# Kernel optimization log

Hardware: AMD Instinct MI355X
Metric: run time of the kernel (lower is better)

Reference implementation:

```python
import jax, jax.numpy as jnp
import numpy as np

B, L, F, P = 128, 256, 4, 4   # dialogs, dialog length, future/past links
IN, H, C = 1024, 256, 7
N = B * L


def _build_edges():
    # same structure as build_intra_graph: self-loop + F future + P past per node
    i = np.arange(L)
    ss, tt = [], []
    for d in range(-P, F + 1):
        j = i + d
        m = (j >= 0) & (j < L)
        ss.append(i[m]); tt.append(j[m])
    s = np.concatenate(ss); t = np.concatenate(tt)
    offs = (np.arange(B) * L)[:, None]
    S = (s[None, :] + offs).ravel()
    T = (t[None, :] + offs).ravel()
    return np.stack([S, T]).astype(np.int32)


def setup_inputs() -> dict:
    key = jax.random.key(0)
    ks = jax.random.split(key, 16)
    ei = _build_edges()
    speakers = np.asarray(jax.random.randint(ks[0], (N,), 0, 2), dtype=np.int32)
    rel = (speakers[ei[0]] * speakers[ei[1]]).astype(np.int32)
    sd_in = 1.0 / np.sqrt(IN)
    sd_h = 1.0 / np.sqrt(H)
    return {
        "input": jax.random.normal(ks[1], (N, IN), jnp.float32),
        "dialog_lengths": jnp.full((B,), L, jnp.int32),
        "speakers": jnp.asarray(speakers),
        "labels": jax.random.randint(ks[2], (N,), 0, C, jnp.int32),
        "edge_index": jnp.asarray(ei),
        "rel_type": jnp.asarray(rel),
        # RGCNConv(IN, H, num_relations=2): per-relation weight, root weight, bias
        "W_rgcn": jax.random.normal(ks[3], (2, IN, H), jnp.float32) * sd_in,
        "W_root": jax.random.normal(ks[4], (IN, H), jnp.float32) * sd_in,
        "b_rgcn": jax.random.normal(ks[5], (H,), jnp.float32) * 0.01,
        # GraphConv(H, H): lin_rel (on aggregated neighbors, with bias), lin_root (no bias)
        "W_rel": jax.random.normal(ks[6], (H, H), jnp.float32) * sd_h,
        "b_rel": jax.random.normal(ks[7], (H,), jnp.float32) * 0.01,
        "W_grt": jax.random.normal(ks[8], (H, H), jnp.float32) * sd_h,
        # skip_con: Linear(IN, H)
        "W_skip": jax.random.normal(ks[9], (IN, H), jnp.float32) * sd_in,
        "b_skip": jax.random.normal(ks[10], (H,), jnp.float32) * 0.01,
        # classify: Linear(H, C)
        "W_cls": jax.random.normal(ks[11], (H, C), jnp.float32) * sd_h,
        "b_cls": jax.random.normal(ks[12], (C,), jnp.float32) * 0.01,
    }


def reference(input, dialog_lengths, speakers, labels, edge_index, rel_type,
              W_rgcn, W_root, b_rgcn, W_rel, b_rel, W_grt,
              W_skip, b_skip, W_cls, b_cls):
    n = input.shape[0]
    src, dst = edge_index[0], edge_index[1]
    seg = jax.ops.segment_sum

    # --- RGCNConv: out_i = x_i @ W_root + b + sum_r mean_{j in N_r(i)} x_j @ W_r
    t = jnp.einsum('ni,rio->rno', input, W_rgcn)      # [2, N, H]
    msg = t[rel_type, src]                            # [E, H] relation-specific messages
    h = input @ W_root + b_rgcn
    for r in range(2):
        m = (rel_type == r).astype(input.dtype)       # [E]
        s = seg(msg * m[:, None], dst, num_segments=n)
        cnt = seg(m, dst, num_segments=n)
        h = h + s / jnp.maximum(cnt, 1.0)[:, None]    # mean aggregation per relation

    # --- GraphConv (aggr='add'): out_i = W_rel @ sum_j h_j + b_rel + W_grt @ h_i
    neigh = seg(h[src], dst, num_segments=n)          # [N, H]
    h2 = neigh @ W_rel + b_rel + h @ W_grt

    # --- skip connection + classifier
    out = (h2 + input @ W_skip + b_skip) @ W_cls + b_cls  # [N, C]

    # --- cross entropy (mean)
    logp = jax.nn.log_softmax(out, axis=-1)
    loss = -jnp.mean(jnp.take_along_axis(logp, labels[:, None].astype(jnp.int32), axis=1))
    return out, loss
```

## Files before the change

### kernel.cpp

```cpp
#include <hip/hip_runtime.h>

#define NN 32768
#define INF 1024
#define HF 256

typedef __bf16 bf16x8 __attribute__((ext_vector_type(8)));
typedef float f32x4 __attribute__((ext_vector_type(4)));
typedef unsigned short u16x8 __attribute__((ext_vector_type(8)));

__device__ __forceinline__ float bf2f(unsigned short u) {
  union { unsigned int i; float f; } v; v.i = ((unsigned int)u) << 16; return v.f;
}
__device__ __forceinline__ unsigned short f2bf(float f) {
  union { float f; unsigned int i; } v; v.f = f;
  unsigned int x = v.i;
  return (unsigned short)((x + 0x7fffu + ((x >> 16) & 1u)) >> 16);
}

__device__ __forceinline__ void ld_lds16(const unsigned short* g, unsigned short* l) {
  __builtin_amdgcn_global_load_lds(
      (__attribute__((address_space(1))) const unsigned int*)g,
      (__attribute__((address_space(3))) unsigned int*)l, 16, 0, 0);
}

__global__ __launch_bounds__(256)
void diagcn_prep(const float* __restrict__ x, const float* __restrict__ Wrgcn,
                 const float* __restrict__ Wroot, const float* __restrict__ Wskip,
                 const float* __restrict__ Wgrt, const float* __restrict__ Wrel,
                 unsigned short* __restrict__ Xbf, unsigned short* __restrict__ WbigT,
                 unsigned short* __restrict__ WsmT, float* __restrict__ loss) {
  int bid = blockIdx.x;
  if (bid < 32768) {
    if (bid == 0 && threadIdx.x == 0) loss[0] = 0.f;
    int idx = bid * 256 + threadIdx.x;
    float4 v = ((const float4*)x)[idx];
    ushort4 u; u.x = f2bf(v.x); u.y = f2bf(v.y); u.z = f2bf(v.z); u.w = f2bf(v.w);
    ((ushort4*)Xbf)[idx] = u;
    return;
  }
  __shared__ float tile[64 * 65];
  int tb = bid - 32768;
  const float* src;
  int k0, ncol0;
  unsigned short* dst;
  int ldd, nrow0;
  if (tb < 256) {
    int tn = tb >> 4, tk = tb & 15;
    int mat = tn >> 2;
    src = (mat == 0) ? Wrgcn : (mat == 1) ? (Wrgcn + 262144) : (mat == 2) ? Wroot : Wskip;
    k0 = tk * 64; ncol0 = (tn & 3) * 64;
    dst = WbigT; ldd = 1024; nrow0 = tn * 64;
  } else {
    int t2 = tb - 256;
    int tn = t2 >> 3, tk = t2 & 7;
    src = (tk < 4) ? Wgrt : Wrel;
    k0 = (tk & 3) * 64; ncol0 = tn * 64;
    dst = WsmT; ldd = 512; nrow0 = tn * 64;
  }
  int kdst0 = (tb < 256) ? k0 : (((tb - 256) & 7) * 64);
  int c = threadIdx.x & 63, rb = threadIdx.x >> 6;
#pragma unroll
  for (int it = 0; it < 16; ++it) {
    int r = rb + it * 4;
    tile[r * 65 + c] = src[(size_t)(k0 + r) * 256 + ncol0 + c];
  }
  __syncthreads();
  int kk = threadIdx.x & 63;
#pragma unroll
  for (int it = 0; it < 16; ++it) {
    int nn = rb + it * 4;
    dst[(size_t)(nrow0 + nn) * ldd + kdst0 + kk] = f2bf(tile[kk * 65 + nn]);
  }
}

template<bool STG, int VM, bool LAST>
__device__ __forceinline__ void g1_tile(int t,
    const unsigned short* __restrict__ gA0, const unsigned short* __restrict__ gB0,
    unsigned short* SH, int w, int abase, int bbase, int sw8,
    bf16x8 (&av)[4], bf16x8 (&bv)[4], bf16x8 (&nav)[4], bf16x8 (&nbv)[4],
    f32x4 (&acc)[8][4]) {
  unsigned short* Ab = SH + ((t & 3) << 14);
  unsigned short* Bb = Ab + 8192;
  bf16x8 av2[4];
#pragma unroll
  for (int i = 0; i < 4; ++i)
    av2[i] = *(const bf16x8*)&Ab[(abase + 64 + i * 16) * 32 + sw8];
  __builtin_amdgcn_sched_barrier(0);
  if (STG) {
    unsigned short* dA = SH + (((t + 3) & 3) << 14) + (w << 10);
    const unsigned short* gA = gA0 + (t + 3) * 32;
    ld_lds16(gA, dA);
    ld_lds16(gA + 16 * 1024, dA + 512);
    unsigned short* dB = SH + (((t + 3) & 3) << 14) + 8192 + (w << 10);
    const unsigned short* gB = gB0 + (t + 3) * 32;
    ld_lds16(gB, dB);
    ld_lds16(gB + 16 * 1024, dB + 512);
  }
  asm volatile("s_waitcnt lgkmcnt(4)");
  __builtin_amdgcn_sched_barrier(0);
  __builtin_amdgcn_s_setprio(1);
#pragma unroll
  for (int i = 0; i < 4; ++i)
#pragma unroll
    for (int j = 0; j < 4; ++j)
      acc[i][j] = __builtin_amdgcn_mfma_f32_16x16x32_bf16(av[i], bv[j], acc[i][j], 0, 0, 0);
  __builtin_amdgcn_s_setprio(0);
  __builtin_amdgcn_sched_barrier(0);
  if constexpr (VM == 8) asm volatile("s_waitcnt vmcnt(8)" ::: "memory");
  else if constexpr (VM == 4) asm volatile("s_waitcnt vmcnt(4)" ::: "memory");
  else if constexpr (VM == 0) asm volatile("s_waitcnt vmcnt(0)" ::: "memory");
  __builtin_amdgcn_s_barrier();
  if constexpr (!LAST) {
    unsigned short* An = SH + (((t + 1) & 3) << 14);
    unsigned short* Bn = An + 8192;
#pragma unroll
    for (int i = 0; i < 4; ++i)
      nav[i] = *(const bf16x8*)&An[(abase + i * 16) * 32 + sw8];
    __builtin_amdgcn_sched_barrier(0);
    asm volatile("s_waitcnt lgkmcnt(4)");
    __builtin_amdgcn_sched_barrier(0);
    __builtin_amdgcn_s_setprio(1);
#pragma unroll
    for (int i = 0; i < 2; ++i)
#pragma unroll
      for (int j = 0; j < 4; ++j)
        acc[4 + i][j] = __builtin_amdgcn_mfma_f32_16x16x32_bf16(av2[i], bv[j], acc[4 + i][j], 0, 0, 0);
    __builtin_amdgcn_s_setprio(0);
    __builtin_amdgcn_sched_barrier(0);
#pragma unroll
    for (int j = 0; j < 4; ++j)
      nbv[j] = *(const bf16x8*)&Bn[(bbase + j * 16) * 32 + sw8];
    __builtin_amdgcn_sched_barrier(0);
    __builtin_amdgcn_s_setprio(1);
#pragma unroll
    for (int i = 2; i < 4; ++i)
#pragma unroll
      for (int j = 0; j < 4; ++j)
        acc[4 + i][j] = __builtin_amdgcn_mfma_f32_16x16x32_bf16(av2[i], bv[j], acc[4 + i][j], 0, 0, 0);
    __builtin_amdgcn_s_setprio(0);
    __builtin_amdgcn_s_barrier();
  } else {
    asm volatile("s_waitcnt lgkmcnt(0)");
    __builtin_amdgcn_sched_barrier(0);
#pragma unroll
    for (int i = 0; i < 4; ++i)
#pragma unroll
      for (int j = 0; j < 4; ++j)
        acc[4 + i][j] = __builtin_amdgcn_mfma_f32_16x16x32_bf16(av2[i], bv[j], acc[4 + i][j], 0, 0, 0);
  }
}

__global__ __launch_bounds__(512, 2)
void diagcn_gemm1(const unsigned short* __restrict__ A, const unsigned short* __restrict__ BT,
                  unsigned short* __restrict__ Y) {
  __shared__ unsigned short SH[65536];
  const int tid = threadIdx.x;
  const int w = tid >> 6, lane = tid & 63;
  const int quad = lane >> 4, l15 = lane & 15;
  const int wm = w >> 2, wn = w & 3;
  const int b = blockIdx.x;
  const int wg = ((b & 7) << 6) + (b >> 3);
  const int m0 = (wg >> 2) << 8;
  const int n0 = (wg & 3) << 8;
  const int abase = wm * 128 + l15;
  const int bbase = wn * 64 + l15;
  const int sw8 = ((quad ^ ((l15 >> 1) & 3)) << 3);
  const int csrc8 = (((lane & 3) ^ ((lane >> 3) & 3)) << 3);
  const unsigned short* gA0 = A + (size_t)(m0 + w * 32 + (lane >> 2)) * 1024 + csrc8;
  const unsigned short* gB0 = BT + (size_t)(n0 + w * 32 + (lane >> 2)) * 1024 + csrc8;

  f32x4 acc[8][4] = {};
  bf16x8 avA[4], bvA[4], avB[4], bvB[4];

#pragma unroll
  for (int tt = 0; tt < 3; ++tt) {
    unsigned short* dA = SH + (tt << 14) + (w << 10);
    ld_lds16(gA0 + tt * 32, dA);
    ld_lds16(gA0 + tt * 32 + 16 * 1024, dA + 512);
    unsigned short* dB = SH + (tt << 14) + 8192 + (w << 10);
    ld_lds16(gB0 + tt * 32, dB);
    ld_lds16(gB0 + tt * 32 + 16 * 1024, dB + 512);
  }
  asm volatile("s_waitcnt vmcnt(8)" ::: "memory");
  __builtin_amdgcn_s_barrier();
#pragma unroll
  for (int i = 0; i < 4; ++i)
    avA[i] = *(const bf16x8*)&SH[(abase + i * 16) * 32 + sw8];
#pragma unroll
  for (int j = 0; j < 4; ++j)
    bvA[j] = *(const bf16x8*)&SH[8192 + (bbase + j * 16) * 32 + sw8];
  __builtin_amdgcn_sched_barrier(0);

#pragma unroll 1
  for (int tt = 0; tt < 14; ++tt) {
    g1_tile<true, 8, false>(2 * tt, gA0, gB0, SH, w, abase, bbase, sw8,
                            avA, bvA, avB, bvB, acc);
    g1_tile<true, 8, false>(2 * tt + 1, gA0, gB0, SH, w, abase, bbase, sw8,
                            avB, bvB, avA, bvA, acc);
  }
  g1_tile<true, 8, false>(28, gA0, gB0, SH, w, abase, bbase, sw8, avA, bvA, avB, bvB, acc);
  g1_tile<false, 4, false>(29, gA0, gB0, SH, w, abase, bbase, sw8, avB, bvB, avA, bvA, acc);
  g1_tile<false, 0, false>(30, gA0, gB0, SH, w, abase, bbase, sw8, avA, bvA, avB, bvB, acc);
  g1_tile<false, -1, true>(31, gA0, gB0, SH, w, abase, bbase, sw8, avB, bvB, avA, bvA, acc);

#pragma unroll
  for (int i = 0; i < 8; ++i)
#pragma unroll
    for (int j = 0; j < 4; ++j) {
      const int row = m0 + wm * 128 + i * 16 + quad * 4;
      const int col = n0 + wn * 64 + j * 16 + l15;
#pragma unroll
      for (int r = 0; r < 4; ++r)
        Y[(size_t)(row + r) * 1024 + col] = f2bf(acc[i][j][r]);
    }
}

__global__ __launch_bounds__(256)
void diagcn_hn(const unsigned short* __restrict__ Y, const int* __restrict__ spk,
               const float* __restrict__ brgcn, unsigned short* __restrict__ A2) {
  __shared__ unsigned short hbuf[72 * 256];
  int b = blockIdx.x;
  int node0 = ((b & 7) << 12) + ((b >> 3) << 6);
  int d0 = node0 & ~255;
  int wv = threadIdx.x >> 6, lane = threadIdx.x & 63;
  int half = lane >> 5, li = lane & 31, c0 = li << 3;
  int slot = wv * 2 + half;

#pragma unroll 1
  for (int pass = 0; pass < 9; ++pass) {
    int idx = pass * 8 + slot;
    int src = node0 - 4 + idx;
    int sc = src < d0 ? d0 : (src > d0 + 255 ? d0 + 255 : src);
    int p = sc & 255;
    int si = spk[sc];
    float a0[8] = {}, a1[8] = {};
    float n0 = 0.f, n1 = 0.f;
#pragma unroll
    for (int d = -4; d <= 4; ++d) {
      int pj = p + d;
      float w = (pj >= 0 && pj < 256) ? 1.f : 0.f;
      int jc = pj < 0 ? 0 : (pj > 255 ? 255 : pj);
      int nj = d0 + jc;
      int rel = si & spk[nj];
      u16x8 v = *(const u16x8*)&Y[(size_t)nj * 1024 + (rel << 8) + c0];
      float w1 = rel ? w : 0.f, w0 = rel ? 0.f : w;
#pragma unroll
      for (int k = 0; k < 8; ++k) {
        float f = bf2f(v[k]);
        a0[k] += f * w0; a1[k] += f * w1;
      }
      n0 += w0; n1 += w1;
    }
    u16x8 vr = *(const u16x8*)&Y[(size_t)sc * 1024 + 512 + c0];
    float i0 = 1.f / fmaxf(n0, 1.f), i1 = 1.f / fmaxf(n1, 1.f);
    u16x8 u;
#pragma unroll
    for (int k = 0; k < 8; ++k)
      u[k] = f2bf(bf2f(vr[k]) + brgcn[c0 + k] + a0[k] * i0 + a1[k] * i1);
    *(u16x8*)&hbuf[idx * 256 + c0] = u;
    if (idx >= 4 && idx < 68)
      *(u16x8*)&A2[(size_t)(node0 + idx - 4) * 512 + c0] = u;
  }
  __syncthreads();

#pragma unroll 1
  for (int pass = 0; pass < 8; ++pass) {
    int idx = pass * 8 + slot;
    int node = node0 + idx;
    int p = node & 255;
    float s[8] = {};
#pragma unroll
    for (int d = -4; d <= 4; ++d) {
      int pj = p + d;
      float w = (pj >= 0 && pj < 256) ? 1.f : 0.f;
      int lidx = idx + 4 + d;
      u16x8 v = *(const u16x8*)&hbuf[lidx * 256 + c0];
#pragma unroll
      for (int k = 0; k < 8; ++k) s[k] += bf2f(v[k]) * w;
    }
    u16x8 u;
#pragma unroll
    for (int k = 0; k < 8; ++k) u[k] = f2bf(s[k]);
    *(u16x8*)&A2[(size_t)node * 512 + 256 + c0] = u;
  }
}

__global__ __launch_bounds__(256)
void diagcn_gemm2(const unsigned short* __restrict__ A, const unsigned short* __restrict__ BT,
                  const unsigned short* __restrict__ Y, const float* __restrict__ Wcls,
                  const float* __restrict__ bcls, const float* __restrict__ brel,
                  const float* __restrict__ bskip, const int* __restrict__ labels,
                  float* __restrict__ out, float* __restrict__ loss) {
  const int K = 512;
  __shared__ unsigned short As[64 * 64];
  __shared__ unsigned short Bs[256 * 64];
  __shared__ float Wc[2312];
  for (int i = threadIdx.x; i < 2312; i += 256) {
    float v;
    if (i < 1792) v = Wcls[i];
    else if (i < 1799) v = bcls[i - 1792];
    else if (i < 1800) v = 0.f;
    else if (i < 2056) v = brel[i - 1800];
    else v = bskip[i - 2056];
    Wc[i] = v;
  }
  const int tid = threadIdx.x;
  const int w = tid >> 6, lane = tid & 63;
  const int quad = lane >> 4, l15 = lane & 15;
  const int b = blockIdx.x;
  const int m0 = (((b & 7) << 6) + (b >> 3)) << 6;
  const int rowg = lane >> 3;
  const int kbsw = (lane & 7) ^ rowg;

  f32x4 acc[16] = {};
  const unsigned short* Abase = A + (size_t)m0 * K + kbsw * 8;
  const unsigned short* Bbase = BT + kbsw * 8;

  for (int k0 = 0; k0 < K; k0 += 64) {
#pragma unroll
    for (int t = 0; t < 2; ++t) {
      int grp = w * 2 + t;
      ld_lds16(Abase + (size_t)(grp * 8 + rowg) * K + k0, &As[grp * 512]);
    }
#pragma unroll
    for (int t = 0; t < 8; ++t) {
      int grp = w * 8 + t;
      ld_lds16(Bbase + (size_t)(grp * 8 + rowg) * K + k0, &Bs[grp * 512]);
    }
    __syncthreads();
#pragma unroll
    for (int ks = 0; ks < 2; ++ks) {
      int kb = ks * 4 + quad;
      int ra = w * 16 + l15;
      bf16x8 av = *(const bf16x8*)&As[ra * 64 + ((kb ^ (ra & 7)) << 3)];
#pragma unroll
      for (int j = 0; j < 16; ++j) {
        int rb2 = j * 16 + l15;
        bf16x8 bv = *(const bf16x8*)&Bs[rb2 * 64 + ((kb ^ (rb2 & 7)) << 3)];
        acc[j] = __builtin_amdgcn_mfma_f32_16x16x32_bf16(av, bv, acc[j], 0, 0, 0);
      }
    }
    __syncthreads();
  }

  float wsum[4][7] = {};
#pragma unroll
  for (int j = 0; j < 16; ++j) {
    int col = j * 16 + l15;
    float bb = Wc[1800 + col] + Wc[2056 + col];
#pragma unroll
    for (int r = 0; r < 4; ++r) {
      int row = m0 + w * 16 + quad * 4 + r;
      float z = acc[j][r] + bb + bf2f(Y[(size_t)row * 1024 + 768 + col]);
#pragma unroll
      for (int c = 0; c < 7; ++c) wsum[r][c] += z * Wc[col * 7 + c];
    }
  }
#pragma unroll
  for (int o = 1; o < 16; o <<= 1)
#pragma unroll
    for (int r = 0; r < 4; ++r)
#pragma unroll
      for (int c = 0; c < 7; ++c) wsum[r][c] += __shfl_xor(wsum[r][c], o, 64);

  float lsum = 0.f;
#pragma unroll
  for (int r = 0; r < 4; ++r) {
    int row = m0 + w * 16 + quad * 4 + r;
    float o7[7], mx = -1e30f;
#pragma unroll
    for (int c = 0; c < 7; ++c) {
      o7[c] = wsum[r][c] + Wc[1792 + c];
      mx = fmaxf(mx, o7[c]);
    }
    if (l15 < 7) out[(size_t)row * 7 + l15] = o7[l15];
    float s = 0.f;
#pragma unroll
    for (int c = 0; c < 7; ++c) s += expf(o7[c] - mx);
    int lab = labels[row];
    lsum += mx + logf(s) - o7[lab];
  }
  lsum += __shfl_xor(lsum, 16, 64);
  lsum += __shfl_xor(lsum, 32, 64);
  if (lane == 0) atomicAdd(loss, lsum * (1.0f / (float)NN));
}

extern "C" void kernel_launch(void* const* d_in, const int* in_sizes, int n_in,
                              void* d_out, int out_size, void* d_ws, size_t ws_size,
                              hipStream_t stream) {
  const float* x      = (const float*)d_in[0];
  const int* speakers = (const int*)d_in[2];
  const int* labels   = (const int*)d_in[3];
  const float* Wrgcn  = (const float*)d_in[6];
  const float* Wroot  = (const float*)d_in[7];
  const float* brgcn  = (const float*)d_in[8];
  const float* Wrel   = (const float*)d_in[9];
  const float* brel   = (const float*)d_in[10];
  const float* Wgrt   = (const float*)d_in[11];
  const float* Wskip  = (const float*)d_in[12];
  const float* bskip  = (const float*)d_in[13];
  const float* Wcls   = (const float*)d_in[14];
  const float* bcls   = (const float*)d_in[15];
  float* out = (float*)d_out;
  float* loss = out + (size_t)NN * 7;

  const size_t OFF_XBF  = 0;
  const size_t OFF_WBIG = 67108864;
  const size_t OFF_WSM  = 69206016;
  const size_t OFF_Y    = 69468160;
  const size_t OFF_A2   = 136577024;
  const size_t NEED     = 170131456;
  if (ws_size < NEED) return;

  char* ws = (char*)d_ws;
  unsigned short* Xbf   = (unsigned short*)(ws + OFF_XBF);
  unsigned short* WbigT = (unsigned short*)(ws + OFF_WBIG);
  unsigned short* WsmT  = (unsigned short*)(ws + OFF_WSM);
  unsigned short* Y     = (unsigned short*)(ws + OFF_Y);
  unsigned short* A2    = (unsigned short*)(ws + OFF_A2);

  diagcn_prep<<<dim3(33056), dim3(256), 0, stream>>>(x, Wrgcn, Wroot, Wskip, Wgrt, Wrel,
                                                     Xbf, WbigT, WsmT, loss);
  diagcn_gemm1<<<dim3(512), dim3(512), 0, stream>>>(Xbf, WbigT, Y);
  diagcn_hn<<<dim3(512), dim3(256), 0, stream>>>(Y, speakers, brgcn, A2);
  diagcn_gemm2<<<dim3(512), dim3(256), 0, stream>>>(A2, WsmT, Y, Wcls, bcls, brel, bskip,
                                                    labels, out, loss);
}
```

Baseline: 369.1 us.

## Fuse fp32-to-bf16 input conversion into GEMM1 A-tile staging

Removes the separate pass that converted the 32768x1024 fp32 input to bf16 in workspace. GEMM1 now loads fp32 A tiles into registers two stages ahead, converts them to bf16 and writes them to LDS itself, while B tiles still use direct global-to-LDS loads. This avoids writing and rereading a 64 MB bf16 copy, at the cost of twice the global read bytes for A inside the GEMM, extra VGPRs and conversion ALU work in the pipelined loop, and reworked waitcnt accounting.

```diff
diff --git a/kernel.cpp b/kernel.cpp
--- a/kernel.cpp
+++ b/kernel.cpp
@@ -24,22 +24,13 @@
 }
 
 __global__ __launch_bounds__(256)
-void diagcn_prep(const float* __restrict__ x, const float* __restrict__ Wrgcn,
-                 const float* __restrict__ Wroot, const float* __restrict__ Wskip,
-                 const float* __restrict__ Wgrt, const float* __restrict__ Wrel,
-                 unsigned short* __restrict__ Xbf, unsigned short* __restrict__ WbigT,
+void diagcn_prep(const float* __restrict__ Wrgcn, const float* __restrict__ Wroot,
+                 const float* __restrict__ Wskip, const float* __restrict__ Wgrt,
+                 const float* __restrict__ Wrel, unsigned short* __restrict__ WbigT,
                  unsigned short* __restrict__ WsmT, float* __restrict__ loss) {
-  int bid = blockIdx.x;
-  if (bid < 32768) {
-    if (bid == 0 && threadIdx.x == 0) loss[0] = 0.f;
-    int idx = bid * 256 + threadIdx.x;
-    float4 v = ((const float4*)x)[idx];
-    ushort4 u; u.x = f2bf(v.x); u.y = f2bf(v.y); u.z = f2bf(v.z); u.w = f2bf(v.w);
-    ((ushort4*)Xbf)[idx] = u;
-    return;
-  }
+  int tb = blockIdx.x;
+  if (tb == 0 && threadIdx.x == 0) loss[0] = 0.f;
   __shared__ float tile[64 * 65];
-  int tb = bid - 32768;
   const float* src;
   int k0, ncol0;
   unsigned short* dst;
@@ -73,30 +64,48 @@
   }
 }
 
-template<bool STG, int VM, bool LAST>
+template<bool WR, bool LDA, bool LDB, int VM, bool LAST>
 __device__ __forceinline__ void g1_tile(int t,
-    const unsigned short* __restrict__ gA0, const unsigned short* __restrict__ gB0,
-    unsigned short* SH, int w, int abase, int bbase, int sw8,
+    const float* __restrict__ gAf, const unsigned short* __restrict__ gB0,
+    unsigned short* SH, int w, int lane, int abase, int bbase, int sw8,
     bf16x8 (&av)[4], bf16x8 (&bv)[4], bf16x8 (&nav)[4], bf16x8 (&nbv)[4],
-    f32x4 (&acc)[8][4]) {
+    f32x4 (&sreg)[4], f32x4 (&acc)[8][4]) {
   unsigned short* Ab = SH + ((t & 3) << 14);
   unsigned short* Bb = Ab + 8192;
+  if constexpr (VM == 2) asm volatile("s_waitcnt vmcnt(2)" ::: "memory");
+  else if constexpr (VM == 0) asm volatile("s_waitcnt vmcnt(0)" ::: "memory");
+  if constexpr (WR) {
+    unsigned short* dA = SH + (((t + 2) & 3) << 14) + (w << 10) + lane * 8;
+    u16x8 p0, p1;
+#pragma unroll
+    for (int k = 0; k < 4; ++k) {
+      p0[k] = f2bf(sreg[0][k]); p0[4 + k] = f2bf(sreg[1][k]);
+      p1[k] = f2bf(sreg[2][k]); p1[4 + k] = f2bf(sreg[3][k]);
+    }
+    *(u16x8*)dA = p0;
+    *(u16x8*)(dA + 512) = p1;
+  }
+  __builtin_amdgcn_sched_barrier(0);
   bf16x8 av2[4];
 #pragma unroll
   for (int i = 0; i < 4; ++i)
     av2[i] = *(const bf16x8*)&Ab[(abase + 64 + i * 16) * 32 + sw8];
   __builtin_amdgcn_sched_barrier(0);
-  if (STG) {
-    unsigned short* dA = SH + (((t + 3) & 3) << 14) + (w << 10);
-    const unsigned short* gA = gA0 + (t + 3) * 32;
-    ld_lds16(gA, dA);
-    ld_lds16(gA + 16 * 1024, dA + 512);
+  if constexpr (LDA) {
+    const float* g = gAf + (t + 3) * 32;
+    sreg[0] = *(const f32x4*)g;
+    sreg[1] = *(const f32x4*)(g + 4);
+    sreg[2] = *(const f32x4*)(g + 16384);
+    sreg[3] = *(const f32x4*)(g + 16388);
+  }
+  if constexpr (LDB) {
     unsigned short* dB = SH + (((t + 3) & 3) << 14) + 8192 + (w << 10);
     const unsigned short* gB = gB0 + (t + 3) * 32;
     ld_lds16(gB, dB);
     ld_lds16(gB + 16 * 1024, dB + 512);
   }
-  asm volatile("s_waitcnt lgkmcnt(4)");
+  if constexpr (WR) asm volatile("s_waitcnt lgkmcnt(6)");
+  else              asm volatile("s_waitcnt lgkmcnt(4)");
   __builtin_amdgcn_sched_barrier(0);
   __builtin_amdgcn_s_setprio(1);
 #pragma unroll
@@ -105,10 +114,6 @@
     for (int j = 0; j < 4; ++j)
       acc[i][j] = __builtin_amdgcn_mfma_f32_16x16x32_bf16(av[i], bv[j], acc[i][j], 0, 0, 0);
   __builtin_amdgcn_s_setprio(0);
-  __builtin_amdgcn_sched_barrier(0);
-  if constexpr (VM == 8) asm volatile("s_waitcnt vmcnt(8)" ::: "memory");
-  else if constexpr (VM == 4) asm volatile("s_waitcnt vmcnt(4)" ::: "memory");
-  else if constexpr (VM == 0) asm volatile("s_waitcnt vmcnt(0)" ::: "memory");
   __builtin_amdgcn_s_barrier();
   if constexpr (!LAST) {
     unsigned short* An = SH + (((t + 1) & 3) << 14);
@@ -151,7 +156,7 @@
 }
 
 __global__ __launch_bounds__(512, 2)
-void diagcn_gemm1(const unsigned short* __restrict__ A, const unsigned short* __restrict__ BT,
+void diagcn_gemm1(const float* __restrict__ X, const unsigned short* __restrict__ BT,
                   unsigned short* __restrict__ Y) {
   __shared__ unsigned short SH[65536];
   const int tid = threadIdx.x;
@@ -166,22 +171,54 @@
   const int bbase = wn * 64 + l15;
   const int sw8 = ((quad ^ ((l15 >> 1) & 3)) << 3);
   const int csrc8 = (((lane & 3) ^ ((lane >> 3) & 3)) << 3);
-  const unsigned short* gA0 = A + (size_t)(m0 + w * 32 + (lane >> 2)) * 1024 + csrc8;
+  const float* gAf = X + (size_t)(m0 + w * 32 + (lane >> 2)) * 1024 + csrc8;
   const unsigned short* gB0 = BT + (size_t)(n0 + w * 32 + (lane >> 2)) * 1024 + csrc8;
 
   f32x4 acc[8][4] = {};
+  f32x4 sreg[4];
   bf16x8 avA[4], bvA[4], avB[4], bvB[4];
 
-#pragma unroll
-  for (int tt = 0; tt < 3; ++tt) {
-    unsigned short* dA = SH + (tt << 14) + (w << 10);
-    ld_lds16(gA0 + tt * 32, dA);
-    ld_lds16(gA0 + tt * 32 + 16 * 1024, dA + 512);
-    unsigned short* dB = SH + (tt << 14) + 8192 + (w << 10);
-    ld_lds16(gB0 + tt * 32, dB);
-    ld_lds16(gB0 + tt * 32 + 16 * 1024, dB + 512);
+  {
+    unsigned short* dA = SH + (w << 10) + lane * 8;
+#pragma unroll
+    for (int tt = 0; tt < 2; ++tt) {
+      const float* g = gAf + tt * 32;
+      sreg[0] = *(const f32x4*)g;
+      sreg[1] = *(const f32x4*)(g + 4);
+      sreg[2] = *(const f32x4*)(g + 16384);
+      sreg[3] = *(const f32x4*)(g + 16388);
+      asm volatile("s_waitcnt vmcnt(0)" ::: "memory");
+      u16x8 p0, p1;
+#pragma unroll
+      for (int k = 0; k < 4; ++k) {
+        p0[k] = f2bf(sreg[0][k]); p0[4 + k] = f2bf(sreg[1][k]);
+        p1[k] = f2bf(sreg[2][k]); p1[4 + k] = f2bf(sreg[3][k]);
+      }
+      unsigned short* d = dA + tt * 16384;
+      *(u16x8*)d = p0;
+      *(u16x8*)(d + 512) = p1;
+    }
+#pragma unroll
+    for (int tt = 0; tt < 2; ++tt) {
+      unsigned short* dB = SH + (tt << 14) + 8192 + (w << 10);
+      ld_lds16(gB0 + tt * 32, dB);
+      ld_lds16(gB0 + tt * 32 + 16 * 1024, dB + 512);
+    }
+    {
+      const float* g = gAf + 2 * 32;
+      sreg[0] = *(const f32x4*)g;
+      sreg[1] = *(const f32x4*)(g + 4);
+      sreg[2] = *(const f32x4*)(g + 16384);
+      sreg[3] = *(const f32x4*)(g + 16388);
+    }
+    {
+      unsigned short* dB = SH + (2 << 14) + 8192 + (w << 10);
+      ld_lds16(gB0 + 2 * 32, dB);
+      ld_lds16(gB0 + 2 * 32 + 16 * 1024, dB + 512);
+    }
   }
   asm volatile("s_waitcnt vmcnt(8)" ::: "memory");
+  asm volatile("s_waitcnt lgkmcnt(0)");
   __builtin_amdgcn_s_barrier();
 #pragma unroll
   for (int i = 0; i < 4; ++i)
@@ -193,15 +230,19 @@
 
 #pragma unroll 1
   for (int tt = 0; tt < 14; ++tt) {
-    g1_tile<true, 8, false>(2 * tt, gA0, gB0, SH, w, abase, bbase, sw8,
-                            avA, bvA, avB, bvB, acc);
-    g1_tile<true, 8, false>(2 * tt + 1, gA0, gB0, SH, w, abase, bbase, sw8,
-                            avB, bvB, avA, bvA, acc);
-  }
-  g1_tile<true, 8, false>(28, gA0, gB0, SH, w, abase, bbase, sw8, avA, bvA, avB, bvB, acc);
-  g1_tile<false, 4, false>(29, gA0, gB0, SH, w, abase, bbase, sw8, avB, bvB, avA, bvA, acc);
-  g1_tile<false, 0, false>(30, gA0, gB0, SH, w, abase, bbase, sw8, avA, bvA, avB, bvB, acc);
-  g1_tile<false, -1, true>(31, gA0, gB0, SH, w, abase, bbase, sw8, avB, bvB, avA, bvA, acc);
+    g1_tile<true, true, true, 2, false>(2 * tt, gAf, gB0, SH, w, lane, abase, bbase, sw8,
+                                        avA, bvA, avB, bvB, sreg, acc);
+    g1_tile<true, true, true, 2, false>(2 * tt + 1, gAf, gB0, SH, w, lane, abase, bbase, sw8,
+                                        avB, bvB, avA, bvA, sreg, acc);
+  }
+  g1_tile<true, true, true, 2, false>(28, gAf, gB0, SH, w, lane, abase, bbase, sw8,
+                                      avA, bvA, avB, bvB, sreg, acc);
+  g1_tile<true, false, false, 2, false>(29, gAf, gB0, SH, w, lane, abase, bbase, sw8,
+                                        avB, bvB, avA, bvA, sreg, acc);
+  g1_tile<false, false, false, 0, false>(30, gAf, gB0, SH, w, lane, abase, bbase, sw8,
+                                         avA, bvA, avB, bvB, sreg, acc);
+  g1_tile<false, false, false, -1, true>(31, gAf, gB0, SH, w, lane, abase, bbase, sw8,
+                                         avB, bvB, avA, bvA, sreg, acc);
 
 #pragma unroll
   for (int i = 0; i < 8; ++i)
@@ -404,24 +445,22 @@
   float* out = (float*)d_out;
   float* loss = out + (size_t)NN * 7;
 
-  const size_t OFF_XBF  = 0;
-  const size_t OFF_WBIG = 67108864;
-  const size_t OFF_WSM  = 69206016;
-  const size_t OFF_Y    = 69468160;
-  const size_t OFF_A2   = 136577024;
-  const size_t NEED     = 170131456;
+  const size_t OFF_WBIG = 0;
+  const size_t OFF_WSM  = 2097152;
+  const size_t OFF_Y    = 2359296;
+  const size_t OFF_A2   = 69468160;
+  const size_t NEED     = 103022592;
   if (ws_size < NEED) return;
 
   char* ws = (char*)d_ws;
-  unsigned short* Xbf   = (unsigned short*)(ws + OFF_XBF);
   unsigned short* WbigT = (unsigned short*)(ws + OFF_WBIG);
   unsigned short* WsmT  = (unsigned short*)(ws + OFF_WSM);
   unsigned short* Y     = (unsigned short*)(ws + OFF_Y);
   unsigned short* A2    = (unsigned short*)(ws + OFF_A2);
 
-  diagcn_prep<<<dim3(33056), dim3(256), 0, stream>>>(x, Wrgcn, Wroot, Wskip, Wgrt, Wrel,
-                                                     Xbf, WbigT, WsmT, loss);
-  diagcn_gemm1<<<dim3(512), dim3(512), 0, stream>>>(Xbf, WbigT, Y);
+  diagcn_prep<<<dim3(288), dim3(256), 0, stream>>>(Wrgcn, Wroot, Wskip, Wgrt, Wrel,
+                                                   WbigT, WsmT, loss);
+  diagcn_gemm1<<<dim3(512), dim3(512), 0, stream>>>(x, WbigT, Y);
   diagcn_hn<<<dim3(512), dim3(256), 0, stream>>>(Y, speakers, brgcn, A2);
   diagcn_gemm2<<<dim3(512), dim3(256), 0, stream>>>(A2, WsmT, Y, Wcls, bcls, brel, bskip,
                                                     labels, out, loss);
```

Result: no change. 376.5 us (+2.0%).
